# Optimization experiments

Hardware: AMD Instinct MI355X
Metric: run time of the kernel (lower is better)

## Reference

```python
import jax, jax.numpy as jnp
import numpy as np

N, E, D, H, K, G = 100000, 1600000, 64, 64, 3, 64


def setup_inputs() -> dict:
    key = jax.random.key(0)
    ks = jax.random.split(key, 16)
    x = jax.random.normal(ks[0], (N, D), dtype=jnp.float32)
    edge_index = jax.random.randint(ks[1], (2, E), 0, N, dtype=jnp.int64)
    batch = jnp.sort(jax.random.randint(ks[2], (N,), 0, G, dtype=jnp.int64))
    s = 0.1
    inp = {
        "x": x, "edge_index": edge_index, "batch": batch,
        # ChebConv weights: [K, Din, Dout] and bias [Dout]
        "w1": jax.random.normal(ks[3], (K, D, H), dtype=jnp.float32) * s,
        "b1": jnp.zeros((H,), jnp.float32),
        "w2": jax.random.normal(ks[4], (K, H, H), dtype=jnp.float32) * s,
        "b2": jnp.zeros((H,), jnp.float32),
        "w3": jax.random.normal(ks[5], (K, H, H), dtype=jnp.float32) * s,
        "b3": jnp.zeros((H,), jnp.float32),
        # BatchNorm affine params
        "g1": jnp.ones((H,), jnp.float32), "be1": jnp.zeros((H,), jnp.float32),
        "g2": jnp.ones((H,), jnp.float32), "be2": jnp.zeros((H,), jnp.float32),
        "g3": jnp.ones((H,), jnp.float32), "be3": jnp.zeros((H,), jnp.float32),
        # shortcut Linear(input_dim, hidden3) and lin1(hidden3, 1)
        "w_sc": jax.random.normal(ks[6], (D, H), dtype=jnp.float32) * s,
        "b_sc": jnp.zeros((H,), jnp.float32),
        "w_lin": jax.random.normal(ks[7], (H, 1), dtype=jnp.float32) * s,
        "b_lin": jnp.zeros((1,), jnp.float32),
    }
    return inp


def _laplacian_norm(row, col, n):
    # PyG ChebConv default: sym normalization, lambda_max=2 -> L_hat = L - I = -D^{-1/2} A D^{-1/2}
    deg = jax.ops.segment_sum(jnp.ones(row.shape[0], jnp.float32), row, num_segments=n)
    dis = jnp.where(deg > 0, jax.lax.rsqrt(jnp.maximum(deg, 1e-12)), 0.0)
    return -dis[row] * dis[col]  # [E]


def _cheb_conv(x, row, col, norm, W, b):
    n = x.shape[0]
    prop = lambda z: jax.ops.segment_sum(norm[:, None] * z[col], row, num_segments=n)
    Tx0 = x
    out = Tx0 @ W[0]
    Tx1 = prop(Tx0)
    out = out + Tx1 @ W[1]
    for k in range(2, W.shape[0]):
        Tx2 = 2.0 * prop(Tx1) - Tx0
        out = out + Tx2 @ W[k]
        Tx0, Tx1 = Tx1, Tx2
    return out + b


def _bn(x, g, b, eps=1e-5):
    mu = jnp.mean(x, axis=0)
    var = jnp.mean(jnp.square(x - mu), axis=0)  # biased, as torch BN training stats
    return (x - mu) * jax.lax.rsqrt(var + eps) * g + b


def reference(x, edge_index, batch, w1, b1, w2, b2, w3, b3,
              g1, be1, g2, be2, g3, be3, w_sc, b_sc, w_lin, b_lin):
    row, col = edge_index[0], edge_index[1]
    norm = _laplacian_norm(row, col, x.shape[0])
    lrelu = lambda h: jax.nn.leaky_relu(h, negative_slope=0.01)
    identity = x
    h = lrelu(_bn(_cheb_conv(x, row, col, norm, w1, b1), g1, be1))
    h = lrelu(_bn(_cheb_conv(h, row, col, norm, w2, b2), g2, be2))
    h = lrelu(_bn(_cheb_conv(h, row, col, norm, w3, b3), g3, be3))
    h = h + (identity @ w_sc + b_sc)
    pooled = jax.ops.segment_max(h, batch, num_segments=G)  # [G, H]
    return pooled @ w_lin + b_lin  # [G, 1]
```

## Files before the change

### kernel.cpp

```cpp
#include <hip/hip_runtime.h>

#define DIV_UP(a,b) (((a)+(b)-1)/(b))

typedef float v4f __attribute__((ext_vector_type(4)));
typedef unsigned short us4 __attribute__((ext_vector_type(4)));
typedef __attribute__((ext_vector_type(8))) short bf16x8;
typedef __attribute__((ext_vector_type(4))) float f32x4;

__device__ __forceinline__ float4 ntload4(const float* p) {
  v4f v = __builtin_nontemporal_load((const v4f*)p);
  return make_float4(v.x, v.y, v.z, v.w);
}

__device__ __forceinline__ unsigned f2key(float f) {
  unsigned u = __float_as_uint(f);
  return (u & 0x80000000u) ? ~u : (u | 0x80000000u);
}
__device__ __forceinline__ float key2f(unsigned u) {
  unsigned b = (u & 0x80000000u) ? (u ^ 0x80000000u) : ~u;
  return __uint_as_float(b);
}

__device__ __forceinline__ unsigned short f2bf(float f) {
  unsigned u = __float_as_uint(f);
  unsigned r = u + 0x7FFFu + ((u >> 16) & 1u);
  return (unsigned short)(r >> 16);
}
__device__ __forceinline__ float bf2f(unsigned short s) {
  return __uint_as_float(((unsigned)s) << 16);
}

__device__ __forceinline__ int swz(int row) {
  return ((row ^ (row >> 3)) & 7) << 3;
}

__global__ void k_scan1(const int* __restrict__ cnt, int* __restrict__ incl,
                        int* __restrict__ bsum, int N) {
  __shared__ int s[1024];
  int t = threadIdx.x;
  int i = blockIdx.x * 1024 + t;
  int v = (i < N) ? cnt[i] : 0;
  s[t] = v;
  __syncthreads();
  for (int off = 1; off < 1024; off <<= 1) {
    int add = (t >= off) ? s[t - off] : 0;
    __syncthreads();
    s[t] += add;
    __syncthreads();
  }
  if (i < N) incl[i] = s[t];
  if (t == 1023) bsum[blockIdx.x] = s[1023];
}

__global__ void k_scan2(const int* __restrict__ bsum, int* __restrict__ bex, int nb) {
  __shared__ int s[128];
  int t = threadIdx.x;
  if (nb <= 128) {
    int v = (t < nb) ? bsum[t] : 0;
    s[t] = v;
    __syncthreads();
    for (int off = 1; off < 128; off <<= 1) {
      int add = (t >= off) ? s[t - off] : 0;
      __syncthreads();
      s[t] += add;
      __syncthreads();
    }
    if (t < nb) bex[t] = s[t] - v;
  } else if (t == 0) {
    int run = 0;
    for (int b = 0; b < nb; ++b) { bex[b] = run; run += bsum[b]; }
  }
}

__global__ void k_scan3(const int* __restrict__ incl, const int* __restrict__ cnt,
                        const int* __restrict__ bex, int* __restrict__ rowptr,
                        float* __restrict__ dis, int N, int E) {
  int i = blockIdx.x * blockDim.x + threadIdx.x;
  if (i < N) {
    int c = cnt[i];
    rowptr[i] = incl[i] - c + bex[i >> 10];
    dis[i] = (c > 0) ? rsqrtf((float)c) : 0.0f;
  }
  if (i == 0) rowptr[N] = E;
}

__device__ __forceinline__ void gemmsc_body(unsigned short* wTsc, unsigned short* x16,
                                            int bid,
                                            const float* __restrict__ X,
                                            const float* __restrict__ W,
                                            const float* __restrict__ bias,
                                            unsigned short* __restrict__ Sbf, int N) {
  int tid = threadIdx.x;
  for (int i4 = tid; i4 < 1024; i4 += 512) {
    int d = i4 >> 4, h4 = i4 & 15;
    float4 v = ((const float4*)W)[i4];
    int colb = h4 * 4;
    wTsc[(colb + 0) * 64 + (d ^ swz(colb + 0))] = f2bf(v.x);
    wTsc[(colb + 1) * 64 + (d ^ swz(colb + 1))] = f2bf(v.y);
    wTsc[(colb + 2) * 64 + (d ^ swz(colb + 2))] = f2bf(v.z);
    wTsc[(colb + 3) * 64 + (d ^ swz(colb + 3))] = f2bf(v.w);
  }
  int rowbase = bid * 128;
  for (int i4 = tid; i4 < 2048; i4 += 512) {
    int r = i4 >> 4, c4 = i4 & 15;
    int row = rowbase + r;
    float4 v = (row < N) ? ntload4(X + (size_t)row * 64 + c4 * 4)
                         : make_float4(0.f, 0.f, 0.f, 0.f);
    us4 pk;
    pk.x = f2bf(v.x); pk.y = f2bf(v.y); pk.z = f2bf(v.z); pk.w = f2bf(v.w);
    *(us4*)&x16[r * 64 + ((c4 * 4) ^ swz(r))] = pk;
  }
  __syncthreads();

  int lane = tid & 63;
  int wv = tid >> 6;
  int lo = lane & 15;
  int hi = lane >> 4;

  f32x4 acc[4];
#pragma unroll
  for (int ct = 0; ct < 4; ++ct) acc[ct] = (f32x4){0.f, 0.f, 0.f, 0.f};

#pragma unroll
  for (int ks = 0; ks < 2; ++ks) {
    int ar = wv * 16 + lo;
    bf16x8 af = *(const bf16x8*)&x16[ar * 64 + ((ks * 32 + hi * 8) ^ swz(ar))];
#pragma unroll
    for (int ct = 0; ct < 4; ++ct) {
      int br = ct * 16 + lo;
      bf16x8 bfr = *(const bf16x8*)&wTsc[br * 64 + ((ks * 32 + hi * 8) ^ swz(br))];
      acc[ct] = __builtin_amdgcn_mfma_f32_16x16x32_bf16(af, bfr, acc[ct], 0, 0, 0);
    }
  }

  float bv[4];
#pragma unroll
  for (int ct = 0; ct < 4; ++ct) bv[ct] = bias[ct * 16 + lo];
  int rowb = rowbase + wv * 16 + hi * 4;
#pragma unroll
  for (int reg = 0; reg < 4; ++reg) {
    int row = rowb + reg;
    if (row < N) {
      size_t o = (size_t)row * 64 + lo;
#pragma unroll
      for (int ct = 0; ct < 4; ++ct)
        __builtin_nontemporal_store(f2bf(acc[ct][reg] + bv[ct]), &Sbf[o + ct * 16]);
    }
  }
}

__device__ __forceinline__ void mfma192_tail(const unsigned short* x16,
                                             const unsigned short* wT,
                                             int rowbase, int tid,
                                             const float* __restrict__ bias,
                                             const float* __restrict__ dis,
                                             unsigned short* __restrict__ A02bf,
                                             unsigned short* __restrict__ Y1bf,
                                             unsigned short* __restrict__ Y2bf,
                                             int N) {
  int lane = tid & 63;
  int wv = tid >> 6;
  int lo = lane & 15;
  int hi = lane >> 4;

  f32x4 acc[12];
#pragma unroll
  for (int ct = 0; ct < 12; ++ct) acc[ct] = (f32x4){0.f, 0.f, 0.f, 0.f};

#pragma unroll
  for (int ks = 0; ks < 2; ++ks) {
    int ar = wv * 16 + lo;
    bf16x8 af = *(const bf16x8*)&x16[ar * 64 + ((ks * 32 + hi * 8) ^ swz(ar))];
#pragma unroll
    for (int ct = 0; ct < 12; ++ct) {
      int br = ct * 16 + lo;
      bf16x8 bfr = *(const bf16x8*)&wT[br * 64 + ((ks * 32 + hi * 8) ^ swz(br))];
      acc[ct] = __builtin_amdgcn_mfma_f32_16x16x32_bf16(af, bfr, acc[ct], 0, 0, 0);
    }
  }

  float bv[4];
#pragma unroll
  for (int ct = 0; ct < 4; ++ct) bv[ct] = bias[ct * 16 + lo];
  int rowb = rowbase + wv * 16 + hi * 4;
#pragma unroll
  for (int reg = 0; reg < 4; ++reg) {
    int row = rowb + reg;
    if (row < N) {
      float dn = dis[row];
      size_t o = (size_t)row * 64 + lo;
#pragma unroll
      for (int ct = 0; ct < 4; ++ct) {
        float o0 = acc[ct][reg] + bv[ct];
        float o1 = acc[ct + 4][reg];
        float o2 = acc[ct + 8][reg];
        A02bf[o + ct * 16] = f2bf(o0 - o2);
        Y1bf[o + ct * 16] = f2bf(o1);
        Y2bf[o + ct * 16] = f2bf(dn * o2);
      }
    }
  }
}

__device__ __forceinline__ void stage_wT(unsigned short* wT,
                                         const float* __restrict__ W, int tid) {
  for (int i4 = tid; i4 < 3072; i4 += 512) {
    int k3 = i4 >> 10, rem = i4 & 1023;
    int d = rem >> 4, h4 = rem & 15;
    float4 v = ((const float4*)W)[i4];
    int colb = k3 * 64 + h4 * 4;
    wT[(colb + 0) * 64 + (d ^ swz(colb + 0))] = f2bf(v.x);
    wT[(colb + 1) * 64 + (d ^ swz(colb + 1))] = f2bf(v.y);
    wT[(colb + 2) * 64 + (d ^ swz(colb + 2))] = f2bf(v.z);
    wT[(colb + 3) * 64 + (d ^ swz(colb + 3))] = f2bf(v.w);
  }
}

__device__ __forceinline__ void gemm192_l0_body(unsigned short* x16, unsigned short* wT,
                                                int bid,
                                                const float* __restrict__ X,
                                                const float* __restrict__ W,
                                                const float* __restrict__ bias,
                                                const float* __restrict__ dis,
                                                unsigned short* __restrict__ A02bf,
                                                unsigned short* __restrict__ Y1bf,
                                                unsigned short* __restrict__ Y2bf,
                                                int N) {
  int tid = threadIdx.x;
  stage_wT(wT, W, tid);
  int rowbase = bid * 128;
  for (int i4 = tid; i4 < 2048; i4 += 512) {
    int r = i4 >> 4, c4 = i4 & 15;
    int row = rowbase + r;
    float4 v = (row < N) ? ntload4(X + (size_t)row * 64 + c4 * 4)
                         : make_float4(0.f, 0.f, 0.f, 0.f);
    us4 pk;
    pk.x = f2bf(v.x); pk.y = f2bf(v.y); pk.z = f2bf(v.z); pk.w = f2bf(v.w);
    *(us4*)&x16[r * 64 + ((c4 * 4) ^ swz(r))] = pk;
  }
  __syncthreads();
  mfma192_tail(x16, wT, rowbase, tid, bias, dis, A02bf, Y1bf, Y2bf, N);
}

__global__ __launch_bounds__(512) void k_fused_a(const float* __restrict__ X,
                                                 const float* __restrict__ W,
                                                 const float* __restrict__ bias,
                                                 unsigned short* __restrict__ Sbf,
                                                 const int* __restrict__ row,
                                                 int* __restrict__ cnt,
                                                 int* __restrict__ eslot,
                                                 unsigned short* __restrict__ Y2bf,
                                                 unsigned short* __restrict__ Vbf,
                                                 unsigned* __restrict__ pooled,
                                                 int N, int E, int NBG, int NC,
                                                 int npool, int q) {
  __shared__ unsigned short wTsc[64 * 64];
  __shared__ unsigned short x16a[128 * 64];
  int bid = blockIdx.x;
  bool isg = (bid % q == 0) && (bid / q < NBG);
  if (isg) {
    gemmsc_body(wTsc, x16a, bid / q, X, W, bias, Sbf, N);
  } else {
    int before = min((bid + q - 1) / q, NBG);
    int oi = bid - before;
    if (oi < NC) {
      int e0 = oi * 2048 + threadIdx.x;
      int r[4], idx[4];
#pragma unroll
      for (int k = 0; k < 4; ++k) {
        int e = e0 + k * 512;
        if (e < E) r[k] = row[e];
      }
#pragma unroll
      for (int k = 0; k < 4; ++k) {
        int e = e0 + k * 512;
        if (e < E) idx[k] = atomicAdd(&cnt[r[k]], 1);
      }
#pragma unroll
      for (int k = 0; k < 4; ++k) {
        int e = e0 + k * 512;
        if (e < E) __builtin_nontemporal_store(idx[k], &eslot[e]);
      }
    } else if (oi == NC) {
      if (threadIdx.x < 64) {
        Y2bf[(size_t)N * 64 + threadIdx.x] = 0;
        Vbf[(size_t)N * 64 + threadIdx.x] = 0;
      }
    } else {
      int i = (oi - NC - 1) * 512 + threadIdx.x;
      if (i < npool) pooled[i] = 0x007FFFFFu;
    }
  }
}

__global__ __launch_bounds__(512) void k_fused_b(const float* __restrict__ X,
                                                 const float* __restrict__ W,
                                                 const float* __restrict__ bias,
                                                 const float* __restrict__ dis,
                                                 unsigned short* __restrict__ A02bf,
                                                 unsigned short* __restrict__ Y1bf,
                                                 unsigned short* __restrict__ Y2bf,
                                                 const int* __restrict__ row,
                                                 const int* __restrict__ col,
                                                 const int* __restrict__ rowptr,
                                                 const int* __restrict__ eslot,
                                                 int* __restrict__ ccol,
                                                 int N, int E, int NBG, int q) {
  __shared__ unsigned short x16b[128 * 64];
  __shared__ unsigned short wTb[192 * 64];
  int bid = blockIdx.x;
  bool isg = (bid % q == 0) && (bid / q < NBG);
  if (isg) {
    gemm192_l0_body(x16b, wTb, bid / q, X, W, bias, dis, A02bf, Y1bf, Y2bf, N);
  } else {
    int before = min((bid + q - 1) / q, NBG);
    int oi = bid - before;
    int e0 = oi * 2048 + threadIdx.x;
    int r[4], c[4], sl[4], base[4];
#pragma unroll
    for (int k = 0; k < 4; ++k) {
      int e = e0 + k * 512;
      if (e < E) { r[k] = row[e]; c[k] = col[e]; sl[k] = eslot[e]; }
    }
#pragma unroll
    for (int k = 0; k < 4; ++k) {
      int e = e0 + k * 512;
      if (e < E) base[k] = rowptr[r[k]];
    }
#pragma unroll
    for (int k = 0; k < 4; ++k) {
      int e = e0 + k * 512;
      if (e < E) ccol[base[k] + sl[k]] = c[k];
    }
  }
}

__global__ __launch_bounds__(512) void k_gemm192(
    const unsigned short* __restrict__ Cbf,
    const float* __restrict__ sums, const float* __restrict__ sumsq,
    const float* __restrict__ g, const float* __restrict__ be,
    const float* __restrict__ W, const float* __restrict__ bias,
    const float* __restrict__ dis,
    unsigned short* __restrict__ A02bf, unsigned short* __restrict__ Y1bf,
    unsigned short* __restrict__ Y2bf, int N) {
  __shared__ unsigned short x16[128 * 64];
  __shared__ unsigned short wT[192 * 64];
  int bid = blockIdx.x;
  int tid = threadIdx.x;

  int cb = (tid & 15) * 4;
  float inv_n = 1.0f / (float)N;
  float scv[4], shv[4];
#pragma unroll
  for (int k = 0; k < 4; ++k) {
    float mu = sums[cb + k] * inv_n;
    float var = sumsq[cb + k] * inv_n - mu * mu;
    float sc = g[cb + k] * rsqrtf(var + 1e-5f);
    scv[k] = sc;
    shv[k] = be[cb + k] - mu * sc;
  }

  stage_wT(wT, W, tid);

  int rowbase = bid * 128;
  for (int i4 = tid; i4 < 2048; i4 += 512) {
    int r = i4 >> 4, c4 = i4 & 15;
    int row = rowbase + r;
    float vx, vy, vz, vw;
    if (row < N) {
      unsigned long long u =
          *(const unsigned long long*)(Cbf + (size_t)row * 64 + c4 * 4);
      vx = bf2f((unsigned short)(u & 0xffffu));
      vy = bf2f((unsigned short)((u >> 16) & 0xffffu));
      vz = bf2f((unsigned short)((u >> 32) & 0xffffu));
      vw = bf2f((unsigned short)(u >> 48));
    } else {
      vx = vy = vz = vw = 0.f;
    }
    float a = vx * scv[0] + shv[0];
    float b = vy * scv[1] + shv[1];
    float c = vz * scv[2] + shv[2];
    float d = vw * scv[3] + shv[3];
    a = (a > 0.f) ? a : 0.01f * a;
    b = (b > 0.f) ? b : 0.01f * b;
    c = (c > 0.f) ? c : 0.01f * c;
    d = (d > 0.f) ? d : 0.01f * d;
    us4 pk;
    pk.x = f2bf(a); pk.y = f2bf(b); pk.z = f2bf(c); pk.w = f2bf(d);
    *(us4*)&x16[r * 64 + ((c4 * 4) ^ swz(r))] = pk;
  }
  __syncthreads();

  mfma192_tail(x16, wT, rowbase, tid, bias, dis, A02bf, Y1bf, Y2bf, N);
}

__device__ __forceinline__ void gather4(int cw, int qtr, int s,
                                        const unsigned long long* z64, float* a) {
#pragma unroll
  for (int u = 0; u < 4; ++u) {
    int c = __shfl(cw, 4 * u + qtr, 64);
    unsigned long long zv = z64[(size_t)c * 16 + s];
    unsigned d0 = (unsigned)zv, d1 = (unsigned)(zv >> 32);
    a[0] += __uint_as_float(d0 << 16);
    a[1] += __uint_as_float(d0 & 0xFFFF0000u);
    a[2] += __uint_as_float(d1 << 16);
    a[3] += __uint_as_float(d1 & 0xFFFF0000u);
  }
}

template <int MODE>
__global__ __launch_bounds__(256) void k_prop4(const int* __restrict__ rowptr,
                                               const int* __restrict__ ccol,
                                               const float* __restrict__ dis,
                                               const unsigned short* __restrict__ zbf,
                                               const unsigned short* __restrict__ inAbf,
                                               unsigned short* __restrict__ outbf,
                                               float* __restrict__ sums,
                                               float* __restrict__ sumsq,
                                               float* __restrict__ zstats,
                                               int N, int nwaves) {
  if (MODE == 1 && blockIdx.x == 0 && threadIdx.x < 128) zstats[threadIdx.x] = 0.f;
  int gw = blockIdx.x * 4 + (threadIdx.x >> 6);
  int lane = threadIdx.x & 63;
  int wid = threadIdx.x >> 6;
  int qtr = lane >> 4;
  int s = lane & 15;
  const unsigned long long* z64 = (const unsigned long long*)zbf;
  const unsigned long long* inA64 = (const unsigned long long*)inAbf;
  unsigned long long* out64 = (unsigned long long*)outbf;
  float st[4] = {0.f, 0.f, 0.f, 0.f}, st2[4] = {0.f, 0.f, 0.f, 0.f};

  int n = gw, beg = 0, end = 0, cl = 0;
  if (n < N) {
    beg = rowptr[n];
    end = rowptr[n + 1];
    cl = ccol[beg + s];
  }
  while (n < N) {
    int nn = n + nwaves;
    int begn = 0, endn = 0;
    if (nn < N) {
      begn = rowptr[nn];
      endn = rowptr[nn + 1];
    }
    float dn = dis[n];
    size_t o = (size_t)n * 16 + s;
    unsigned long long av = 0;
    if (qtr == 0) av = inA64[o];
    float a[4] = {0.f, 0.f, 0.f, 0.f};
    {
      int c16 = (beg + s < end) ? cl : N;
      gather4(c16, qtr, s, z64, a);
    }
    for (int j = beg + 16; j < end; j += 16) {
      int jj = j + s;
      int c = ccol[jj];
      c = (jj < end) ? c : N;
      gather4(c, qtr, s, z64, a);
    }
    int cln = 0;
    if (nn < N) cln = ccol[begn + s];
#pragma unroll
    for (int k = 0; k < 4; ++k) {
      a[k] += __shfl_xor(a[k], 16, 64);
      a[k] += __shfl_xor(a[k], 32, 64);
    }
    if (qtr == 0) {
      unsigned b0 = (unsigned)av, b1 = (unsigned)(av >> 32);
      float x0 = __uint_as_float(b0 << 16);
      float x1 = __uint_as_float(b0 & 0xFFFF0000u);
      float x2 = __uint_as_float(b1 << 16);
      float x3 = __uint_as_float(b1 & 0xFFFF0000u);
      if (MODE == 1) {
        float v0 = dn * (x0 - 2.f * dn * a[0]);
        float v1 = dn * (x1 - 2.f * dn * a[1]);
        float v2 = dn * (x2 - 2.f * dn * a[2]);
        float v3 = dn * (x3 - 2.f * dn * a[3]);
        unsigned lo = (unsigned)f2bf(v0) | ((unsigned)f2bf(v1) << 16);
        unsigned hi = (unsigned)f2bf(v2) | ((unsigned)f2bf(v3) << 16);
        out64[o] = (unsigned long long)lo | ((unsigned long long)hi << 32);
      } else {
        float v0 = x0 - dn * a[0];
        float v1 = x1 - dn * a[1];
        float v2 = x2 - dn * a[2];
        float v3 = x3 - dn * a[3];
        unsigned lo = (unsigned)f2bf(v0) | ((unsigned)f2bf(v1) << 16);
        unsigned hi = (unsigned)f2bf(v2) | ((unsigned)f2bf(v3) << 16);
        out64[o] = (unsigned long long)lo | ((unsigned long long)hi << 32);
        st[0] += v0; st2[0] = fmaf(v0, v0, st2[0]);
        st[1] += v1; st2[1] = fmaf(v1, v1, st2[1]);
        st[2] += v2; st2[2] = fmaf(v2, v2, st2[2]);
        st[3] += v3; st2[3] = fmaf(v3, v3, st2[3]);
      }
    }
    n = nn; beg = begn; end = endn; cl = cln;
  }
  if (MODE == 2) {
    __shared__ float red[2][4][64];
    if (qtr == 0) {
#pragma unroll
      for (int k = 0; k < 4; ++k) {
        red[0][wid][4 * s + k] = st[k];
        red[1][wid][4 * s + k] = st2[k];
      }
    }
    __syncthreads();
    if (wid == 0) {
      float a = red[0][0][lane] + red[0][1][lane] + red[0][2][lane] + red[0][3][lane];
      float b = red[1][0][lane] + red[1][1][lane] + red[1][2][lane] + red[1][3][lane];
      atomicAdd(&sums[lane], a);
      atomicAdd(&sumsq[lane], b);
    }
  }
}

__global__ void k_bnpool(const unsigned short* __restrict__ Cbf,
                         const float* __restrict__ sums, const float* __restrict__ sumsq,
                         const float* __restrict__ g, const float* __restrict__ be,
                         const unsigned short* __restrict__ Sbf,
                         const int* __restrict__ batch,
                         unsigned* __restrict__ pooled, int N) {
  __shared__ float sc_s[64], sh_s[64];
  if (threadIdx.x < 64) {
    int h = threadIdx.x;
    float inv_n = 1.0f / (float)N;
    float mu = sums[h] * inv_n;
    float var = sumsq[h] * inv_n - mu * mu;
    float sc = g[h] * rsqrtf(var + 1e-5f);
    sc_s[h] = sc;
    sh_s[h] = be[h] - mu * sc;
  }
  __syncthreads();
  int t = threadIdx.x;
  int h = t & 63;
  int rsub = t >> 6;
  int base = blockIdx.x * 64;
  float sc = sc_s[h], sh = sh_s[h];
  int cur_g = -1;
  unsigned best = 0;
  for (int i = 0; i < 16; ++i) {
    int n = base + rsub + 4 * i;
    if (n >= N) break;
    int gidx = batch[n];
    size_t o = (size_t)n * 64 + h;
    float a = bf2f(__builtin_nontemporal_load(&Cbf[o])) * sc + sh;
    a = (a > 0.f) ? a : 0.01f * a;
    a += bf2f(__builtin_nontemporal_load(&Sbf[o]));
    unsigned k = f2key(a);
    if (gidx != cur_g) {
      if (cur_g >= 0) atomicMax(&pooled[cur_g * 64 + h], best);
      cur_g = gidx;
      best = k;
    } else {
      best = max(best, k);
    }
  }
  if (cur_g >= 0) atomicMax(&pooled[cur_g * 64 + h], best);
}

__global__ void k_final(const unsigned* __restrict__ pooled, const float* __restrict__ w_lin,
                        const float* __restrict__ b_lin, float* __restrict__ out) {
  int g = blockIdx.x;
  int h = threadIdx.x;
  float v = key2f(pooled[g * 64 + h]) * w_lin[h];
  for (int off = 32; off > 0; off >>= 1) v += __shfl_down(v, off, 64);
  if (h == 0) out[g] = v + b_lin[0];
}

extern "C" void kernel_launch(void* const* d_in, const int* in_sizes, int n_in,
                              void* d_out, int out_size, void* d_ws, size_t ws_size,
                              hipStream_t stream) {
  const float* x = (const float*)d_in[0];
  const int* ei = (const int*)d_in[1];
  const int* batch = (const int*)d_in[2];
  const float* w1 = (const float*)d_in[3];
  const float* b1 = (const float*)d_in[4];
  const float* w2 = (const float*)d_in[5];
  const float* b2 = (const float*)d_in[6];
  const float* w3 = (const float*)d_in[7];
  const float* b3 = (const float*)d_in[8];
  const float* g1 = (const float*)d_in[9];
  const float* be1 = (const float*)d_in[10];
  const float* g2 = (const float*)d_in[11];
  const float* be2 = (const float*)d_in[12];
  const float* g3 = (const float*)d_in[13];
  const float* be3 = (const float*)d_in[14];
  const float* w_sc = (const float*)d_in[15];
  const float* b_sc = (const float*)d_in[16];
  const float* w_lin = (const float*)d_in[17];
  const float* b_lin = (const float*)d_in[18];

  int N = in_sizes[0] / 64;
  int E = in_sizes[1] / 2;
  int G = out_size;
  const int* row = ei;
  const int* col = ei + E;

  char* p = (char*)d_ws;
  auto carve = [&](size_t bytes) -> void* {
    void* r = (void*)p;
    p += (bytes + 255) & ~(size_t)255;
    return r;
  };
  int* cnt = (int*)carve((size_t)N * 4);
  float* dis = (float*)carve((size_t)N * 4);
  int* rowptr = (int*)carve((size_t)(N + 1) * 4);
  int* eslot = (int*)carve((size_t)E * 4);
  int* incl = (int*)carve((size_t)N * 4);
  int* bsum = (int*)carve(1024);
  int* bex = (int*)carve(1024);
  int* ccol = (int*)carve((size_t)(E + 64) * 4);
  unsigned short* Sbf = (unsigned short*)carve((size_t)N * 64 * 2);
  unsigned short* A02bf = (unsigned short*)carve((size_t)N * 64 * 2);
  unsigned short* Y1bf = (unsigned short*)carve((size_t)N * 64 * 2);
  unsigned short* Y2bf = (unsigned short*)carve((size_t)(N + 1) * 64 * 2);
  unsigned short* Vbf = (unsigned short*)carve((size_t)(N + 1) * 64 * 2);
  unsigned short* Cbf = (unsigned short*)carve((size_t)N * 64 * 2);
  float* stats = (float*)carve(256 * 4);
  unsigned* pooled = (unsigned*)carve((size_t)G * 64 * 4);

  int NBG = DIV_UP(N, 128);
  int NC = DIV_UP(E, 2048);
  int npool = G * 64;
  int NPI = DIV_UP(npool, 512);

  int TA = NBG + NC + 1 + NPI;
  int qa = (NBG > 1) ? (TA - 1) / (NBG - 1) : 1;
  if (qa < 1) qa = 1;
  int TB = NBG + NC;
  int qb = (NBG > 1) ? (TB - 1) / (NBG - 1) : 1;
  if (qb < 1) qb = 1;

  hipMemsetAsync(cnt, 0, (size_t)N * 4, stream);
  k_fused_a<<<TA, 512, 0, stream>>>(x, w_sc, b_sc, Sbf, row, cnt, eslot,
                                    Y2bf, Vbf, pooled, N, E, NBG, NC, npool, qa);
  int nb = DIV_UP(N, 1024);
  k_scan1<<<nb, 1024, 0, stream>>>(cnt, incl, bsum, N);
  k_scan2<<<1, 128, 0, stream>>>(bsum, bex, nb);
  k_scan3<<<DIV_UP(N, 256), 256, 0, stream>>>(incl, cnt, bex, rowptr, dis, N, E);
  k_fused_b<<<TB, 512, 0, stream>>>(x, w1, b1, dis, A02bf, Y1bf, Y2bf,
                                    row, col, rowptr, eslot, ccol, N, E, NBG, qb);

  const float* Ws[3] = {w1, w2, w3};
  const float* bs[3] = {b1, b2, b3};
  const float* gs[3] = {g1, g2, g3};
  const float* bes[3] = {be1, be2, be3};

  const int PBLK = 2048;
  const int NWAVE = PBLK * 4;
  for (int l = 0; l < 3; ++l) {
    if (l > 0)
      k_gemm192<<<NBG, 512, 0, stream>>>(Cbf, stats, stats + 64, gs[l - 1], bes[l - 1],
                                         Ws[l], bs[l], dis, A02bf, Y1bf, Y2bf, N);
    k_prop4<1><<<PBLK, 256, 0, stream>>>(rowptr, ccol, dis, Y2bf, Y1bf,
                                         Vbf, nullptr, nullptr, stats, N, NWAVE);
    k_prop4<2><<<PBLK, 256, 0, stream>>>(rowptr, ccol, dis, Vbf, A02bf,
                                         Cbf, stats, stats + 64, nullptr, N, NWAVE);
  }

  k_bnpool<<<DIV_UP(N, 64), 256, 0, stream>>>(Cbf, stats, stats + 64, g3, be3,
                                              Sbf, batch, pooled, N);
  k_final<<<G, 64, 0, stream>>>(pooled, w_lin, b_lin, (float*)d_out);
}
```

Baseline: 628.3 us.

## Bucket CSR rows by column quarter and gather in phases across seven rows

```diff
diff --git a/kernel.cpp b/kernel.cpp
--- a/kernel.cpp
+++ b/kernel.cpp
@@ -35,11 +35,11 @@
 }
 
 __global__ void k_scan1(const int* __restrict__ cnt, int* __restrict__ incl,
-                        int* __restrict__ bsum, int N) {
+                        int* __restrict__ bsum, int M) {
   __shared__ int s[1024];
   int t = threadIdx.x;
   int i = blockIdx.x * 1024 + t;
-  int v = (i < N) ? cnt[i] : 0;
+  int v = (i < M) ? cnt[i] : 0;
   s[t] = v;
   __syncthreads();
   for (int off = 1; off < 1024; off <<= 1) {
@@ -48,18 +48,18 @@
     s[t] += add;
     __syncthreads();
   }
-  if (i < N) incl[i] = s[t];
+  if (i < M) incl[i] = s[t];
   if (t == 1023) bsum[blockIdx.x] = s[1023];
 }
 
 __global__ void k_scan2(const int* __restrict__ bsum, int* __restrict__ bex, int nb) {
-  __shared__ int s[128];
+  __shared__ int s[512];
   int t = threadIdx.x;
-  if (nb <= 128) {
+  if (nb <= 512) {
     int v = (t < nb) ? bsum[t] : 0;
     s[t] = v;
     __syncthreads();
-    for (int off = 1; off < 128; off <<= 1) {
+    for (int off = 1; off < 512; off <<= 1) {
       int add = (t >= off) ? s[t - off] : 0;
       __syncthreads();
       s[t] += add;
@@ -72,16 +72,17 @@
   }
 }
 
-__global__ void k_scan3(const int* __restrict__ incl, const int* __restrict__ cnt,
-                        const int* __restrict__ bex, int* __restrict__ rowptr,
-                        float* __restrict__ dis, int N, int E) {
+__global__ void k_scan3(const int* __restrict__ incl, const int* __restrict__ cnt4,
+                        const int* __restrict__ bex, int* __restrict__ rowptr4,
+                        float* __restrict__ dis, int N, int M, int E) {
   int i = blockIdx.x * blockDim.x + threadIdx.x;
+  if (i < M) rowptr4[i] = incl[i] - cnt4[i] + bex[i >> 10];
   if (i < N) {
-    int c = cnt[i];
-    rowptr[i] = incl[i] - c + bex[i >> 10];
+    int4 c4 = *(const int4*)&cnt4[4 * i];
+    int c = c4.x + c4.y + c4.z + c4.w;
     dis[i] = (c > 0) ? rsqrtf((float)c) : 0.0f;
   }
-  if (i == 0) rowptr[N] = E;
+  if (i == 0) rowptr4[M] = E;
 }
 
 __device__ __forceinline__ void gemmsc_body(unsigned short* wTsc, unsigned short* x16,
@@ -247,13 +248,14 @@
                                                  const float* __restrict__ bias,
                                                  unsigned short* __restrict__ Sbf,
                                                  const int* __restrict__ row,
-                                                 int* __restrict__ cnt,
+                                                 const int* __restrict__ col,
+                                                 int* __restrict__ cnt4,
                                                  int* __restrict__ eslot,
                                                  unsigned short* __restrict__ Y2bf,
                                                  unsigned short* __restrict__ Vbf,
                                                  unsigned* __restrict__ pooled,
                                                  int N, int E, int NBG, int NC,
-                                                 int npool, int q) {
+                                                 int npool, int q, int shift) {
   __shared__ unsigned short wTsc[64 * 64];
   __shared__ unsigned short x16a[128 * 64];
   int bid = blockIdx.x;
@@ -265,16 +267,16 @@
     int oi = bid - before;
     if (oi < NC) {
       int e0 = oi * 2048 + threadIdx.x;
-      int r[4], idx[4];
+      int r[4], c[4], idx[4];
 #pragma unroll
       for (int k = 0; k < 4; ++k) {
         int e = e0 + k * 512;
-        if (e < E) r[k] = row[e];
+        if (e < E) { r[k] = row[e]; c[k] = col[e]; }
       }
 #pragma unroll
       for (int k = 0; k < 4; ++k) {
         int e = e0 + k * 512;
-        if (e < E) idx[k] = atomicAdd(&cnt[r[k]], 1);
+        if (e < E) idx[k] = atomicAdd(&cnt4[r[k] * 4 + (c[k] >> shift)], 1);
       }
 #pragma unroll
       for (int k = 0; k < 4; ++k) {
@@ -302,10 +304,11 @@
                                                  unsigned short* __restrict__ Y2bf,
                                                  const int* __restrict__ row,
                                                  const int* __restrict__ col,
-                                                 const int* __restrict__ rowptr,
+                                                 const int* __restrict__ rowptr4,
                                                  const int* __restrict__ eslot,
                                                  int* __restrict__ ccol,
-                                                 int N, int E, int NBG, int q) {
+                                                 int N, int E, int NBG, int q,
+                                                 int shift) {
   __shared__ unsigned short x16b[128 * 64];
   __shared__ unsigned short wTb[192 * 64];
   int bid = blockIdx.x;
@@ -325,7 +328,7 @@
 #pragma unroll
     for (int k = 0; k < 4; ++k) {
       int e = e0 + k * 512;
-      if (e < E) base[k] = rowptr[r[k]];
+      if (e < E) base[k] = rowptr4[r[k] * 4 + (c[k] >> shift)];
     }
 #pragma unroll
     for (int k = 0; k < 4; ++k) {
@@ -394,22 +397,9 @@
   mfma192_tail(x16, wT, rowbase, tid, bias, dis, A02bf, Y1bf, Y2bf, N);
 }
 
-__device__ __forceinline__ void gather4(int cw, int qtr, int s,
-                                        const unsigned long long* z64, float* a) {
-#pragma unroll
-  for (int u = 0; u < 4; ++u) {
-    int c = __shfl(cw, 4 * u + qtr, 64);
-    unsigned long long zv = z64[(size_t)c * 16 + s];
-    unsigned d0 = (unsigned)zv, d1 = (unsigned)(zv >> 32);
-    a[0] += __uint_as_float(d0 << 16);
-    a[1] += __uint_as_float(d0 & 0xFFFF0000u);
-    a[2] += __uint_as_float(d1 << 16);
-    a[3] += __uint_as_float(d1 & 0xFFFF0000u);
-  }
-}
-
+#define MAXR 7
 template <int MODE>
-__global__ __launch_bounds__(256) void k_prop4(const int* __restrict__ rowptr,
+__global__ __launch_bounds__(256) void k_prop4(const int* __restrict__ rowptr4,
                                                const int* __restrict__ ccol,
                                                const float* __restrict__ dis,
                                                const unsigned short* __restrict__ zbf,
@@ -430,70 +420,75 @@
   unsigned long long* out64 = (unsigned long long*)outbf;
   float st[4] = {0.f, 0.f, 0.f, 0.f}, st2[4] = {0.f, 0.f, 0.f, 0.f};
 
-  int n = gw, beg = 0, end = 0, cl = 0;
-  if (n < N) {
-    beg = rowptr[n];
-    end = rowptr[n + 1];
-    cl = ccol[beg + s];
-  }
-  while (n < N) {
-    int nn = n + nwaves;
-    int begn = 0, endn = 0;
-    if (nn < N) {
-      begn = rowptr[nn];
-      endn = rowptr[nn + 1];
-    }
-    float dn = dis[n];
-    size_t o = (size_t)n * 16 + s;
-    unsigned long long av = 0;
-    if (qtr == 0) av = inA64[o];
-    float a[4] = {0.f, 0.f, 0.f, 0.f};
-    {
-      int c16 = (beg + s < end) ? cl : N;
-      gather4(c16, qtr, s, z64, a);
-    }
-    for (int j = beg + 16; j < end; j += 16) {
-      int jj = j + s;
-      int c = ccol[jj];
-      c = (jj < end) ? c : N;
-      gather4(c, qtr, s, z64, a);
-    }
-    int cln = 0;
-    if (nn < N) cln = ccol[begn + s];
-#pragma unroll
-    for (int k = 0; k < 4; ++k) {
-      a[k] += __shfl_xor(a[k], 16, 64);
-      a[k] += __shfl_xor(a[k], 32, 64);
-    }
-    if (qtr == 0) {
-      unsigned b0 = (unsigned)av, b1 = (unsigned)(av >> 32);
-      float x0 = __uint_as_float(b0 << 16);
-      float x1 = __uint_as_float(b0 & 0xFFFF0000u);
-      float x2 = __uint_as_float(b1 << 16);
-      float x3 = __uint_as_float(b1 & 0xFFFF0000u);
-      if (MODE == 1) {
-        float v0 = dn * (x0 - 2.f * dn * a[0]);
-        float v1 = dn * (x1 - 2.f * dn * a[1]);
-        float v2 = dn * (x2 - 2.f * dn * a[2]);
-        float v3 = dn * (x3 - 2.f * dn * a[3]);
-        unsigned lo = (unsigned)f2bf(v0) | ((unsigned)f2bf(v1) << 16);
-        unsigned hi = (unsigned)f2bf(v2) | ((unsigned)f2bf(v3) << 16);
-        out64[o] = (unsigned long long)lo | ((unsigned long long)hi << 32);
-      } else {
-        float v0 = x0 - dn * a[0];
-        float v1 = x1 - dn * a[1];
-        float v2 = x2 - dn * a[2];
-        float v3 = x3 - dn * a[3];
-        unsigned lo = (unsigned)f2bf(v0) | ((unsigned)f2bf(v1) << 16);
-        unsigned hi = (unsigned)f2bf(v2) | ((unsigned)f2bf(v3) << 16);
-        out64[o] = (unsigned long long)lo | ((unsigned long long)hi << 32);
-        st[0] += v0; st2[0] = fmaf(v0, v0, st2[0]);
-        st[1] += v1; st2[1] = fmaf(v1, v1, st2[1]);
-        st[2] += v2; st2[2] = fmaf(v2, v2, st2[2]);
-        st[3] += v3; st2[3] = fmaf(v3, v3, st2[3]);
-      }
-    }
-    n = nn; beg = begn; end = endn; cl = cln;
+  for (int n0 = gw; n0 < N; n0 += nwaves * MAXR) {
+    float acc[MAXR][4];
+#pragma unroll
+    for (int ri = 0; ri < MAXR; ++ri) {
+      acc[ri][0] = 0.f; acc[ri][1] = 0.f; acc[ri][2] = 0.f; acc[ri][3] = 0.f;
+    }
+#pragma unroll 1
+    for (int ph = 0; ph < 4; ++ph) {
+#pragma unroll
+      for (int ri = 0; ri < MAXR; ++ri) {
+        int n = n0 + ri * nwaves;
+        if (n < N) {
+          int beg = rowptr4[4 * n + ph];
+          int end = rowptr4[4 * n + ph + 1];
+          for (int j = beg; j < end; j += 4) {
+            int jq = j + qtr;
+            int c = ccol[jq];
+            c = (jq < end) ? c : N;
+            unsigned long long zv = z64[(size_t)c * 16 + s];
+            unsigned d0 = (unsigned)zv, d1 = (unsigned)(zv >> 32);
+            acc[ri][0] += __uint_as_float(d0 << 16);
+            acc[ri][1] += __uint_as_float(d0 & 0xFFFF0000u);
+            acc[ri][2] += __uint_as_float(d1 << 16);
+            acc[ri][3] += __uint_as_float(d1 & 0xFFFF0000u);
+          }
+        }
+      }
+    }
+#pragma unroll
+    for (int ri = 0; ri < MAXR; ++ri) {
+      int n = n0 + ri * nwaves;
+      if (n >= N) continue;
+      float a0 = acc[ri][0], a1 = acc[ri][1], a2 = acc[ri][2], a3 = acc[ri][3];
+      a0 += __shfl_xor(a0, 16, 64); a0 += __shfl_xor(a0, 32, 64);
+      a1 += __shfl_xor(a1, 16, 64); a1 += __shfl_xor(a1, 32, 64);
+      a2 += __shfl_xor(a2, 16, 64); a2 += __shfl_xor(a2, 32, 64);
+      a3 += __shfl_xor(a3, 16, 64); a3 += __shfl_xor(a3, 32, 64);
+      float dn = dis[n];
+      if (qtr == 0) {
+        size_t o = (size_t)n * 16 + s;
+        unsigned long long av = inA64[o];
+        unsigned b0 = (unsigned)av, b1 = (unsigned)(av >> 32);
+        float x0 = __uint_as_float(b0 << 16);
+        float x1 = __uint_as_float(b0 & 0xFFFF0000u);
+        float x2 = __uint_as_float(b1 << 16);
+        float x3 = __uint_as_float(b1 & 0xFFFF0000u);
+        if (MODE == 1) {
+          float v0 = dn * (x0 - 2.f * dn * a0);
+          float v1 = dn * (x1 - 2.f * dn * a1);
+          float v2 = dn * (x2 - 2.f * dn * a2);
+          float v3 = dn * (x3 - 2.f * dn * a3);
+          unsigned lo = (unsigned)f2bf(v0) | ((unsigned)f2bf(v1) << 16);
+          unsigned hi = (unsigned)f2bf(v2) | ((unsigned)f2bf(v3) << 16);
+          out64[o] = (unsigned long long)lo | ((unsigned long long)hi << 32);
+        } else {
+          float v0 = x0 - dn * a0;
+          float v1 = x1 - dn * a1;
+          float v2 = x2 - dn * a2;
+          float v3 = x3 - dn * a3;
+          unsigned lo = (unsigned)f2bf(v0) | ((unsigned)f2bf(v1) << 16);
+          unsigned hi = (unsigned)f2bf(v2) | ((unsigned)f2bf(v3) << 16);
+          out64[o] = (unsigned long long)lo | ((unsigned long long)hi << 32);
+          st[0] += v0; st2[0] = fmaf(v0, v0, st2[0]);
+          st[1] += v1; st2[1] = fmaf(v1, v1, st2[1]);
+          st[2] += v2; st2[2] = fmaf(v2, v2, st2[2]);
+          st[3] += v3; st2[3] = fmaf(v3, v3, st2[3]);
+        }
+      }
+    }
   }
   if (MODE == 2) {
     __shared__ float red[2][4][64];
@@ -596,19 +591,23 @@
   const int* row = ei;
   const int* col = ei + E;
 
+  int shift = 0;
+  while ((4 << shift) < N) shift++;
+
+  int N4 = 4 * N;
   char* p = (char*)d_ws;
   auto carve = [&](size_t bytes) -> void* {
     void* r = (void*)p;
     p += (bytes + 255) & ~(size_t)255;
     return r;
   };
-  int* cnt = (int*)carve((size_t)N * 4);
+  int* cnt4 = (int*)carve((size_t)N4 * 4);
   float* dis = (float*)carve((size_t)N * 4);
-  int* rowptr = (int*)carve((size_t)(N + 1) * 4);
+  int* rowptr4 = (int*)carve((size_t)(N4 + 1) * 4);
   int* eslot = (int*)carve((size_t)E * 4);
-  int* incl = (int*)carve((size_t)N * 4);
-  int* bsum = (int*)carve(1024);
-  int* bex = (int*)carve(1024);
+  int* incl = (int*)carve((size_t)N4 * 4);
+  int* bsum = (int*)carve(4096);
+  int* bex = (int*)carve(4096);
   int* ccol = (int*)carve((size_t)(E + 64) * 4);
   unsigned short* Sbf = (unsigned short*)carve((size_t)N * 64 * 2);
   unsigned short* A02bf = (unsigned short*)carve((size_t)N * 64 * 2);
@@ -631,30 +630,33 @@
   int qb = (NBG > 1) ? (TB - 1) / (NBG - 1) : 1;
   if (qb < 1) qb = 1;
 
-  hipMemsetAsync(cnt, 0, (size_t)N * 4, stream);
-  k_fused_a<<<TA, 512, 0, stream>>>(x, w_sc, b_sc, Sbf, row, cnt, eslot,
-                                    Y2bf, Vbf, pooled, N, E, NBG, NC, npool, qa);
-  int nb = DIV_UP(N, 1024);
-  k_scan1<<<nb, 1024, 0, stream>>>(cnt, incl, bsum, N);
-  k_scan2<<<1, 128, 0, stream>>>(bsum, bex, nb);
-  k_scan3<<<DIV_UP(N, 256), 256, 0, stream>>>(incl, cnt, bex, rowptr, dis, N, E);
+  hipMemsetAsync(cnt4, 0, (size_t)N4 * 4, stream);
+  k_fused_a<<<TA, 512, 0, stream>>>(x, w_sc, b_sc, Sbf, row, col, cnt4, eslot,
+                                    Y2bf, Vbf, pooled, N, E, NBG, NC, npool, qa,
+                                    shift);
+  int nb = DIV_UP(N4, 1024);
+  k_scan1<<<nb, 1024, 0, stream>>>(cnt4, incl, bsum, N4);
+  k_scan2<<<1, 512, 0, stream>>>(bsum, bex, nb);
+  k_scan3<<<DIV_UP(N4, 256), 256, 0, stream>>>(incl, cnt4, bex, rowptr4, dis,
+                                               N, N4, E);
   k_fused_b<<<TB, 512, 0, stream>>>(x, w1, b1, dis, A02bf, Y1bf, Y2bf,
-                                    row, col, rowptr, eslot, ccol, N, E, NBG, qb);
+                                    row, col, rowptr4, eslot, ccol, N, E, NBG, qb,
+                                    shift);
 
   const float* Ws[3] = {w1, w2, w3};
   const float* bs[3] = {b1, b2, b3};
   const float* gs[3] = {g1, g2, g3};
   const float* bes[3] = {be1, be2, be3};
 
-  const int PBLK = 2048;
+  const int PBLK = 4096;
   const int NWAVE = PBLK * 4;
   for (int l = 0; l < 3; ++l) {
     if (l > 0)
       k_gemm192<<<NBG, 512, 0, stream>>>(Cbf, stats, stats + 64, gs[l - 1], bes[l - 1],
                                          Ws[l], bs[l], dis, A02bf, Y1bf, Y2bf, N);
-    k_prop4<1><<<PBLK, 256, 0, stream>>>(rowptr, ccol, dis, Y2bf, Y1bf,
+    k_prop4<1><<<PBLK, 256, 0, stream>>>(rowptr4, ccol, dis, Y2bf, Y1bf,
                                          Vbf, nullptr, nullptr, stats, N, NWAVE);
-    k_prop4<2><<<PBLK, 256, 0, stream>>>(rowptr, ccol, dis, Vbf, A02bf,
+    k_prop4<2><<<PBLK, 256, 0, stream>>>(rowptr4, ccol, dis, Vbf, A02bf,
                                          Cbf, stats, stats + 64, nullptr, N, NWAVE);
   }
 
```

Result: slower. 1.148 ms (+82.7%).
